# Kernel tuning notes

Hardware: AMD Instinct MI355X
Metric: run time of the kernel (lower is better)

Reference implementation:

```python
import jax, jax.numpy as jnp
import numpy as np

D_MODEL = 1024
NUM_HEADS = 16
DEPTH = D_MODEL // NUM_HEADS


def setup_inputs() -> dict:
    key = jax.random.key(0)
    ks = jax.random.split(key, 9)
    B, S = 2, 2048
    scale = 1.0 / np.sqrt(D_MODEL)
    x = jax.random.normal(ks[0], (B, S, D_MODEL), dtype=jnp.float32)
    wq = jax.random.normal(ks[1], (D_MODEL, D_MODEL), dtype=jnp.float32) * scale
    wk = jax.random.normal(ks[2], (D_MODEL, D_MODEL), dtype=jnp.float32) * scale
    wv = jax.random.normal(ks[3], (D_MODEL, D_MODEL), dtype=jnp.float32) * scale
    wo = jax.random.normal(ks[4], (D_MODEL, D_MODEL), dtype=jnp.float32) * scale
    bq = jnp.zeros((D_MODEL,), dtype=jnp.float32)
    bk = jnp.zeros((D_MODEL,), dtype=jnp.float32)
    bv = jnp.zeros((D_MODEL,), dtype=jnp.float32)
    bo = jnp.zeros((D_MODEL,), dtype=jnp.float32)
    return {"x": x, "wq": wq, "bq": bq, "wk": wk, "bk": bk,
            "wv": wv, "bv": bv, "wo": wo, "bo": bo}


def _split_heads(t):
    # [B, S, D] -> [B, H, S, depth]
    B, S, _ = t.shape
    return t.reshape(B, S, NUM_HEADS, DEPTH).transpose(0, 2, 1, 3)


def reference(x, wq, bq, wk, bk, wv, bv, wo, bo):
    q = _split_heads(x @ wq + bq)
    k = _split_heads(x @ wk + bk)
    v = _split_heads(x @ wv + bv)
    # scaled dot-product attention with materialized [B,H,S,S] scores
    logits = jnp.einsum("bhqd,bhkd->bhqk", q, k) / jnp.sqrt(
        jnp.asarray(DEPTH, dtype=x.dtype))
    attn = jax.nn.softmax(logits, axis=-1)
    out = jnp.einsum("bhqk,bhkd->bhqd", attn, v)
    B, _, S, _ = out.shape
    concat = out.transpose(0, 2, 1, 3).reshape(B, S, D_MODEL)
    return concat @ wo + bo
```

## Files before the change

kernel.cpp:

```cpp
#include <hip/hip_runtime.h>
#include <hip/hip_bf16.h>
#include <stdint.h>

typedef unsigned short u16;
typedef __attribute__((ext_vector_type(8))) short short8;
typedef __attribute__((ext_vector_type(4))) float f32x4;

__device__ __forceinline__ float bf2f(u16 u) {
    union { uint32_t u; float f; } v; v.u = ((uint32_t)u) << 16; return v.f;
}
__device__ __forceinline__ u16 f2bf(float f) {
    union { float f; uint32_t u; } v; v.f = f;
    uint32_t r = (v.u + 0x7fffu + ((v.u >> 16) & 1u)) >> 16;
    return (u16)r;
}
__device__ __forceinline__ uint32_t pkbf(float a, float b) {
    union { __hip_bfloat162 h; uint32_t w; } u;
    u.h = __float22bfloat162_rn(float2{a, b});
    return u.w;
}
__device__ __forceinline__ void store_out(u16* p, float v) { *p = f2bf(v); }
__device__ __forceinline__ void store_out(float* p, float v) { *p = v; }

__device__ __forceinline__ void async_ld16(const u16* g, u16* l) {
    __builtin_amdgcn_global_load_lds(
        (const __attribute__((address_space(1))) void*)g,
        (__attribute__((address_space(3))) void*)l, 16, 0, 0);
}

__global__ void prep(const float* __restrict__ x,
                     const float* __restrict__ w0, const float* __restrict__ w1,
                     const float* __restrict__ w2,
                     u16* __restrict__ xb, u16* __restrict__ wT) {
    const int z = blockIdx.z;
    __shared__ u16 tile[32][33];
    if (z >= 3) {
        int blk = (z - 3) * 1024 + blockIdx.y * 32 + blockIdx.x;
        int tid = threadIdx.y * 32 + threadIdx.x;
        int i = (blk * 256 + tid) * 8;
        float4 a = *(const float4*)(x + i);
        float4 b = *(const float4*)(x + i + 4);
        union { uint32_t w[4]; uint4 v; } o;
        o.w[0] = pkbf(a.x, a.y); o.w[1] = pkbf(a.z, a.w);
        o.w[2] = pkbf(b.x, b.y); o.w[3] = pkbf(b.z, b.w);
        *(uint4*)(xb + i) = o.v;
        return;
    }
    const float* in = (z == 0) ? w0 : (z == 1) ? w1 : w2;
    u16* o = wT + (size_t)z * 1024 * 1024;
    int xx = blockIdx.x * 32 + threadIdx.x;
    int y0 = blockIdx.y * 32;
#pragma unroll
    for (int j = threadIdx.y; j < 32; j += 8)
        tile[j][threadIdx.x] = f2bf(in[(size_t)(y0 + j) * 1024 + xx]);
    __syncthreads();
    int ox = blockIdx.y * 32 + threadIdx.x;
    int oy0 = blockIdx.x * 32;
#pragma unroll
    for (int j = threadIdx.y; j < 32; j += 8)
        o[(size_t)(oy0 + j) * 1024 + ox] = tile[threadIdx.x][j];
}

__global__ void transpose1(const float* __restrict__ w, u16* __restrict__ out) {
    __shared__ u16 tile[32][33];
    int x = blockIdx.x * 32 + threadIdx.x;
    int y0 = blockIdx.y * 32;
#pragma unroll
    for (int j = threadIdx.y; j < 32; j += 8)
        tile[j][threadIdx.x] = f2bf(w[(size_t)(y0 + j) * 1024 + x]);
    __syncthreads();
    int ox = blockIdx.y * 32 + threadIdx.x;
    int oy0 = blockIdx.x * 32;
#pragma unroll
    for (int j = threadIdx.y; j < 32; j += 8)
        out[(size_t)(oy0 + j) * 1024 + ox] = tile[threadIdx.x][j];
}

#define GBM 128
#define GBN 128
#define GBK 32

template <typename OutT>
__global__ __launch_bounds__(256) void gemm_bt(
    const u16* __restrict__ A, int lda,
    const u16* __restrict__ BT, int ldb,
    const float* __restrict__ bias0, const float* __restrict__ bias1,
    const float* __restrict__ bias2,
    OutT* __restrict__ C, int ldc, int K) {
    __shared__ __align__(16) u16 As[2][GBM * GBK];
    __shared__ __align__(16) u16 Bs[2][GBN * GBK];

    const int tid = threadIdx.x;
    const int wave = tid >> 6, lane = tid & 63;
    const int quad = lane >> 4, l16 = lane & 15;
    const int wr = wave >> 1, wc = wave & 1;

    int bx = blockIdx.x, by = blockIdx.y;
    if (gridDim.x == 24 && gridDim.y == 32) {
        const int wgid = blockIdx.x + blockIdx.y * 24;
        const int xcd = wgid & 7, t = wgid >> 3;
        bx = (xcd & 1) * 12 + t % 12;
        by = (xcd >> 1) * 8 + t / 12;
    }
    const int m0 = by * GBM, n0 = bx * GBN;

    const int seg = n0 >> 10;
    const float* bsel = (seg == 0) ? bias0 : (seg == 1) ? bias1 : bias2;

    f32x4 acc[4][4] = {};

    const int srow = tid >> 2;
    const int scol = (tid & 3) * 8;
    const u16* Ag0 = A + (size_t)(m0 + srow) * lda + scol;
    const u16* Ag1 = Ag0 + (size_t)64 * lda;
    const u16* Bg0 = BT + (size_t)(n0 + srow) * ldb + scol;
    const u16* Bg1 = Bg0 + (size_t)64 * ldb;
    const int woff = wave << 9;

    async_ld16(Ag0, As[0] + woff);
    async_ld16(Ag1, As[0] + woff + 64 * GBK);
    async_ld16(Bg0, Bs[0] + woff);
    async_ld16(Bg1, Bs[0] + woff + 64 * GBK);

    int cur = 0;
    for (int kb = 0; kb < K; kb += GBK) {
        __syncthreads();

        if (kb + GBK < K) {
            const int nxt = cur ^ 1;
            async_ld16(Ag0 + kb + GBK, As[nxt] + woff);
            async_ld16(Ag1 + kb + GBK, As[nxt] + woff + 64 * GBK);
            async_ld16(Bg0 + kb + GBK, Bs[nxt] + woff);
            async_ld16(Bg1 + kb + GBK, Bs[nxt] + woff + 64 * GBK);
        }

        short8 af[4], bf[4];
#pragma unroll
        for (int mt = 0; mt < 4; mt++)
            af[mt] = *(const short8*)(As[cur] + (wr * 64 + mt * 16 + l16) * GBK + quad * 8);
#pragma unroll
        for (int nt = 0; nt < 4; nt++)
            bf[nt] = *(const short8*)(Bs[cur] + (wc * 64 + nt * 16 + l16) * GBK + quad * 8);
#pragma unroll
        for (int mt = 0; mt < 4; mt++)
#pragma unroll
            for (int nt = 0; nt < 4; nt++)
                acc[mt][nt] = __builtin_amdgcn_mfma_f32_16x16x32_bf16(
                    af[mt], bf[nt], acc[mt][nt], 0, 0, 0);
        cur ^= 1;
    }

#pragma unroll
    for (int nt = 0; nt < 4; nt++) {
        int col = n0 + wc * 64 + nt * 16 + l16;
        float bv = bsel[col & 1023];
#pragma unroll
        for (int mt = 0; mt < 4; mt++) {
            int row = m0 + wr * 64 + mt * 16 + quad * 4;
#pragma unroll
            for (int r = 0; r < 4; r++)
                store_out(&C[(size_t)(row + r) * ldc + col], acc[mt][nt][r] + bv);
        }
    }
}

__global__ __launch_bounds__(256) void gemm_bt64(
    const u16* __restrict__ A, int lda,
    const u16* __restrict__ BT, int ldb,
    const float* __restrict__ bias,
    float* __restrict__ C, int ldc, int K) {
    __shared__ __align__(16) u16 As[2][64 * GBK];
    __shared__ __align__(16) u16 Bs[2][128 * GBK];

    const int tid = threadIdx.x;
    const int wave = tid >> 6, lane = tid & 63;
    const int quad = lane >> 4, l16 = lane & 15;

    int bx = blockIdx.x, by = blockIdx.y;
    if (gridDim.x == 8 && gridDim.y == 64) {
        const int wgid = blockIdx.x + blockIdx.y * 8;
        const int xcd = wgid & 7, t = wgid >> 3;
        bx = t & 7;
        by = (xcd << 3) + (t >> 3);
    }
    const int m0 = by * 64, n0 = bx * 128;

    f32x4 acc[4][2] = {};

    const int srow = tid >> 2;
    const int scol = (tid & 3) * 8;
    const u16* Ag0 = A + (size_t)(m0 + srow) * lda + scol;
    const u16* Bg0 = BT + (size_t)(n0 + srow) * ldb + scol;
    const u16* Bg1 = Bg0 + (size_t)64 * ldb;
    const int woff = wave << 9;

    async_ld16(Ag0, As[0] + woff);
    async_ld16(Bg0, Bs[0] + woff);
    async_ld16(Bg1, Bs[0] + woff + 64 * GBK);

    int cur = 0;
    for (int kb = 0; kb < K; kb += GBK) {
        __syncthreads();

        if (kb + GBK < K) {
            const int nxt = cur ^ 1;
            async_ld16(Ag0 + kb + GBK, As[nxt] + woff);
            async_ld16(Bg0 + kb + GBK, Bs[nxt] + woff);
            async_ld16(Bg1 + kb + GBK, Bs[nxt] + woff + 64 * GBK);
        }

        short8 af[4], bf[2];
#pragma unroll
        for (int mt = 0; mt < 4; mt++)
            af[mt] = *(const short8*)(As[cur] + (mt * 16 + l16) * GBK + quad * 8);
#pragma unroll
        for (int nt = 0; nt < 2; nt++)
            bf[nt] = *(const short8*)(Bs[cur] + (wave * 32 + nt * 16 + l16) * GBK + quad * 8);
#pragma unroll
        for (int mt = 0; mt < 4; mt++)
#pragma unroll
            for (int nt = 0; nt < 2; nt++)
                acc[mt][nt] = __builtin_amdgcn_mfma_f32_16x16x32_bf16(
                    af[mt], bf[nt], acc[mt][nt], 0, 0, 0);
        cur ^= 1;
    }

#pragma unroll
    for (int nt = 0; nt < 2; nt++) {
        int col = n0 + wave * 32 + nt * 16 + l16;
        float bv = bias[col & 1023];
#pragma unroll
        for (int mt = 0; mt < 4; mt++) {
            int row = m0 + mt * 16 + quad * 4;
#pragma unroll
            for (int r = 0; r < 4; r++)
                C[(size_t)(row + r) * ldc + col] = acc[mt][nt][r] + bv;
        }
    }
}

#define SEQ 2048
#define BQT 128
#define BKV 128
#define LDK 72
#define LDKV 136

__global__ __launch_bounds__(256) void attn(u16* __restrict__ QKV) {
    __shared__ __align__(16) u16 Ks[BKV * LDK];
    __shared__ __align__(16) u16 Vs[64 * LDKV];

    const int tid = threadIdx.x;
    const int wave = tid >> 6, lane = tid & 63;
    const int quad = lane >> 4, l16 = lane & 15;
    const int h = blockIdx.y, bb = blockIdx.z;
    const int q0 = blockIdx.x * BQT;
    const size_t tok0 = (size_t)bb * SEQ;

    const u16* Qb = QKV + tok0 * 3072 + h * 64;
    const u16* Kb = QKV + tok0 * 3072 + 1024 + h * 64;
    const u16* Vb = QKV + tok0 * 3072 + 2048 + h * 64;

    const float cs = 0.18033688011112042f;

    int qr[2];
    qr[0] = q0 + wave * 16 + l16;
    qr[1] = qr[0] + 64;
    short8 aq[2][2];
#pragma unroll
    for (int s = 0; s < 2; s++) {
        union { short8 v; u16 u[8]; uint32_t w[4]; } qa, qb;
        qa.v = *(const short8*)(Qb + (size_t)qr[s] * 3072 + quad * 8);
        qb.v = *(const short8*)(Qb + (size_t)qr[s] * 3072 + 32 + quad * 8);
#pragma unroll
        for (int j = 0; j < 4; j++) {
            qa.w[j] = pkbf(bf2f(qa.u[2 * j]) * cs, bf2f(qa.u[2 * j + 1]) * cs);
            qb.w[j] = pkbf(bf2f(qb.u[2 * j]) * cs, bf2f(qb.u[2 * j + 1]) * cs);
        }
        aq[s][0] = qa.v; aq[s][1] = qb.v;
    }

    f32x4 o[2][4] = {};
    f32x4 o_l[2] = {};

    const short8 vone = {16256, 16256, 16256, 16256,
                         16256, 16256, 16256, 16256};

    const int srow = tid >> 2;
    const int scc = (tid & 3) * 16;
    const int pr = tid & 63;
    const int dg = wave;

    const u16* kg = Kb + (size_t)srow * 3072 + scc;
    const u16* vg = Vb + (size_t)(2 * pr) * 3072 + dg * 16;

    const int kvb = 2 * pr;
    const int kvp = (kvb & 96) | (((kvb >> 2) & 3) << 3) |
                    (((kvb >> 4) & 1) << 2) | (kvb & 3);

    uint4 k0r = *(const uint4*)(kg);
    uint4 k1r = *(const uint4*)(kg + 8);
    uint4 k2r = *(const uint4*)(kg + (size_t)64 * 3072);
    uint4 k3r = *(const uint4*)(kg + (size_t)64 * 3072 + 8);
    uint4 va0 = *(const uint4*)(vg);
    uint4 va1 = *(const uint4*)(vg + 8);
    uint4 vb0 = *(const uint4*)(vg + 3072);
    uint4 vb1 = *(const uint4*)(vg + 3072 + 8);

    for (int j0 = 0; j0 < SEQ; j0 += BKV) {
        *(uint4*)(Ks + srow * LDK + scc) = k0r;
        *(uint4*)(Ks + srow * LDK + scc + 8) = k1r;
        *(uint4*)(Ks + (srow + 64) * LDK + scc) = k2r;
        *(uint4*)(Ks + (srow + 64) * LDK + scc + 8) = k3r;
        {
            union { uint4 v[2]; u16 u[16]; } a, b;
            a.v[0] = va0; a.v[1] = va1; b.v[0] = vb0; b.v[1] = vb1;
#pragma unroll
            for (int j = 0; j < 16; j++) {
                uint32_t w = (uint32_t)a.u[j] | ((uint32_t)b.u[j] << 16);
                *(uint32_t*)(Vs + (dg * 16 + j) * LDKV + kvp) = w;
            }
        }
        __syncthreads();

        if (j0 + BKV < SEQ) {
            size_t off = (size_t)(j0 + BKV) * 3072;
            k0r = *(const uint4*)(kg + off);
            k1r = *(const uint4*)(kg + off + 8);
            k2r = *(const uint4*)(kg + off + (size_t)64 * 3072);
            k3r = *(const uint4*)(kg + off + (size_t)64 * 3072 + 8);
            va0 = *(const uint4*)(vg + off);
            va1 = *(const uint4*)(vg + off + 8);
            vb0 = *(const uint4*)(vg + off + 3072);
            vb1 = *(const uint4*)(vg + off + 3072 + 8);
        }

        f32x4 st[2][8];
#pragma unroll
        for (int kkt = 0; kkt < 8; kkt++) {
            f32x4 s0 = {}, s1 = {};
#pragma unroll
            for (int k2 = 0; k2 < 2; k2++) {
                short8 ak = *(const short8*)(Ks + (kkt * 16 + l16) * LDK + k2 * 32 + quad * 8);
                s0 = __builtin_amdgcn_mfma_f32_16x16x32_bf16(ak, aq[0][k2], s0, 0, 0, 0);
                s1 = __builtin_amdgcn_mfma_f32_16x16x32_bf16(ak, aq[1][k2], s1, 0, 0, 0);
            }
            st[0][kkt] = s0; st[1][kkt] = s1;
        }

#pragma unroll
        for (int s = 0; s < 2; s++)
#pragma unroll
            for (int kkt = 0; kkt < 8; kkt++)
#pragma unroll
                for (int r = 0; r < 4; r++)
                    st[s][kkt][r] = __builtin_amdgcn_exp2f(st[s][kkt][r]);

#pragma unroll
        for (int tt = 0; tt < 4; tt++) {
            union { uint32_t w[4]; short8 v; } bp0, bp1;
            bp0.w[0] = pkbf(st[0][2 * tt][0], st[0][2 * tt][1]);
            bp0.w[1] = pkbf(st[0][2 * tt][2], st[0][2 * tt][3]);
            bp0.w[2] = pkbf(st[0][2 * tt + 1][0], st[0][2 * tt + 1][1]);
            bp0.w[3] = pkbf(st[0][2 * tt + 1][2], st[0][2 * tt + 1][3]);
            bp1.w[0] = pkbf(st[1][2 * tt][0], st[1][2 * tt][1]);
            bp1.w[1] = pkbf(st[1][2 * tt][2], st[1][2 * tt][3]);
            bp1.w[2] = pkbf(st[1][2 * tt + 1][0], st[1][2 * tt + 1][1]);
            bp1.w[3] = pkbf(st[1][2 * tt + 1][2], st[1][2 * tt + 1][3]);

            o_l[0] = __builtin_amdgcn_mfma_f32_16x16x32_bf16(vone, bp0.v, o_l[0], 0, 0, 0);
            o_l[1] = __builtin_amdgcn_mfma_f32_16x16x32_bf16(vone, bp1.v, o_l[1], 0, 0, 0);
#pragma unroll
            for (int dt = 0; dt < 4; dt++) {
                short8 av = *(const short8*)(Vs + (dt * 16 + l16) * LDKV +
                                             tt * 32 + quad * 8);
                o[0][dt] = __builtin_amdgcn_mfma_f32_16x16x32_bf16(av, bp0.v, o[0][dt], 0, 0, 0);
                o[1][dt] = __builtin_amdgcn_mfma_f32_16x16x32_bf16(av, bp1.v, o[1][dt], 0, 0, 0);
            }
        }

        __syncthreads();
    }

#pragma unroll
    for (int s = 0; s < 2; s++) {
        const float inv_l = 1.0f / o_l[s][0];
        u16* orow = QKV + (tok0 + qr[s]) * 3072 + h * 64;
#pragma unroll
        for (int dt = 0; dt < 4; dt++) {
            uint32_t w0 = pkbf(o[s][dt][0] * inv_l, o[s][dt][1] * inv_l);
            uint32_t w1 = pkbf(o[s][dt][2] * inv_l, o[s][dt][3] * inv_l);
            uint2 w = {w0, w1};
            *(uint2*)(orow + dt * 16 + quad * 4) = w;
        }
    }
}

extern "C" void kernel_launch(void* const* d_in, const int* in_sizes, int n_in,
                              void* d_out, int out_size, void* d_ws, size_t ws_size,
                              hipStream_t stream) {
    const float* x  = (const float*)d_in[0];
    const float* wq = (const float*)d_in[1];
    const float* bq = (const float*)d_in[2];
    const float* wk = (const float*)d_in[3];
    const float* bk = (const float*)d_in[4];
    const float* wv = (const float*)d_in[5];
    const float* bv = (const float*)d_in[6];
    const float* wo = (const float*)d_in[7];
    const float* bo = (const float*)d_in[8];
    (void)in_sizes; (void)n_in; (void)out_size; (void)ws_size;

    u16* QKV = (u16*)d_ws;
    u16* wT  = QKV + (size_t)4096 * 3072;
    u16* xb  = wT + (size_t)3 * 1024 * 1024;
    u16* woT = xb;

    prep<<<dim3(32, 32, 5), dim3(32, 8), 0, stream>>>(x, wq, wk, wv, xb, wT);
    gemm_bt<u16><<<dim3(24, 32), 256, 0, stream>>>(xb, 1024, wT, 1024, bq, bk, bv,
                                                   QKV, 3072, 1024);
    transpose1<<<dim3(32, 32), dim3(32, 8), 0, stream>>>(wo, woT);
    attn<<<dim3(16, 16, 2), 256, 0, stream>>>(QKV);
    gemm_bt64<<<dim3(8, 64), 256, 0, stream>>>(QKV, 3072, woT, 1024, bo,
                                               (float*)d_out, 1024, 1024);
}
```

Baseline: 200.7 us.

## Split attention block across 8 waves with one query tile per wave

The attention kernel now launches 512 threads per block, and each of the 8 waves owns a single 16-row query tile instead of two. K/V staging is spread across twice as many threads, so each thread loads half as much. The aim is more waves in flight to hide MFMA and exp latency, with fewer registers per thread. In exchange each K/V tile held in LDS is reused by fewer query tiles per wave, and the per-thread instruction-level parallelism drops.

```diff
diff --git a/kernel.cpp b/kernel.cpp
--- a/kernel.cpp
+++ b/kernel.cpp
@@ -245,7 +245,7 @@
 #define LDK 72
 #define LDKV 136
 
-__global__ __launch_bounds__(256) void attn(u16* __restrict__ QKV) {
+__global__ __launch_bounds__(512, 2) void attn(u16* __restrict__ QKV) {
     __shared__ __align__(16) u16 Ks[BKV * LDK];
     __shared__ __align__(16) u16 Vs[64 * LDKV];
 
@@ -262,36 +262,32 @@
 
     const float cs = 0.18033688011112042f;
 
-    int qr[2];
-    qr[0] = q0 + wave * 16 + l16;
-    qr[1] = qr[0] + 64;
-    short8 aq[2][2];
-#pragma unroll
-    for (int s = 0; s < 2; s++) {
+    const int qr = q0 + wave * 16 + l16;
+    short8 aq[2];
+    {
         union { short8 v; u16 u[8]; uint32_t w[4]; } qa, qb;
-        qa.v = *(const short8*)(Qb + (size_t)qr[s] * 3072 + quad * 8);
-        qb.v = *(const short8*)(Qb + (size_t)qr[s] * 3072 + 32 + quad * 8);
+        qa.v = *(const short8*)(Qb + (size_t)qr * 3072 + quad * 8);
+        qb.v = *(const short8*)(Qb + (size_t)qr * 3072 + 32 + quad * 8);
 #pragma unroll
         for (int j = 0; j < 4; j++) {
             qa.w[j] = pkbf(bf2f(qa.u[2 * j]) * cs, bf2f(qa.u[2 * j + 1]) * cs);
             qb.w[j] = pkbf(bf2f(qb.u[2 * j]) * cs, bf2f(qb.u[2 * j + 1]) * cs);
         }
-        aq[s][0] = qa.v; aq[s][1] = qb.v;
-    }
-
-    f32x4 o[2][4] = {};
-    f32x4 o_l[2] = {};
+        aq[0] = qa.v; aq[1] = qb.v;
+    }
+
+    f32x4 o[4] = {};
+    f32x4 o_l = {};
 
     const short8 vone = {16256, 16256, 16256, 16256,
                          16256, 16256, 16256, 16256};
 
     const int srow = tid >> 2;
     const int scc = (tid & 3) * 16;
-    const int pr = tid & 63;
-    const int dg = wave;
-
+    const int pr = lane;
+    const int dgv = wave;
     const u16* kg = Kb + (size_t)srow * 3072 + scc;
-    const u16* vg = Vb + (size_t)(2 * pr) * 3072 + dg * 16;
+    const u16* vg = Vb + (size_t)(2 * pr) * 3072 + dgv * 8;
 
     const int kvb = 2 * pr;
     const int kvp = (kvb & 96) | (((kvb >> 2) & 3) << 3) |
@@ -299,25 +295,19 @@
 
     uint4 k0r = *(const uint4*)(kg);
     uint4 k1r = *(const uint4*)(kg + 8);
-    uint4 k2r = *(const uint4*)(kg + (size_t)64 * 3072);
-    uint4 k3r = *(const uint4*)(kg + (size_t)64 * 3072 + 8);
     uint4 va0 = *(const uint4*)(vg);
-    uint4 va1 = *(const uint4*)(vg + 8);
     uint4 vb0 = *(const uint4*)(vg + 3072);
-    uint4 vb1 = *(const uint4*)(vg + 3072 + 8);
 
     for (int j0 = 0; j0 < SEQ; j0 += BKV) {
         *(uint4*)(Ks + srow * LDK + scc) = k0r;
         *(uint4*)(Ks + srow * LDK + scc + 8) = k1r;
-        *(uint4*)(Ks + (srow + 64) * LDK + scc) = k2r;
-        *(uint4*)(Ks + (srow + 64) * LDK + scc + 8) = k3r;
         {
-            union { uint4 v[2]; u16 u[16]; } a, b;
-            a.v[0] = va0; a.v[1] = va1; b.v[0] = vb0; b.v[1] = vb1;
-#pragma unroll
-            for (int j = 0; j < 16; j++) {
+            union { uint4 v; u16 u[8]; } a, b;
+            a.v = va0; b.v = vb0;
+#pragma unroll
+            for (int j = 0; j < 8; j++) {
                 uint32_t w = (uint32_t)a.u[j] | ((uint32_t)b.u[j] << 16);
-                *(uint32_t*)(Vs + (dg * 16 + j) * LDKV + kvp) = w;
+                *(uint32_t*)(Vs + (dgv * 8 + j) * LDKV + kvp) = w;
             }
         }
         __syncthreads();
@@ -326,69 +316,55 @@
             size_t off = (size_t)(j0 + BKV) * 3072;
             k0r = *(const uint4*)(kg + off);
             k1r = *(const uint4*)(kg + off + 8);
-            k2r = *(const uint4*)(kg + off + (size_t)64 * 3072);
-            k3r = *(const uint4*)(kg + off + (size_t)64 * 3072 + 8);
             va0 = *(const uint4*)(vg + off);
-            va1 = *(const uint4*)(vg + off + 8);
             vb0 = *(const uint4*)(vg + off + 3072);
-            vb1 = *(const uint4*)(vg + off + 3072 + 8);
-        }
-
-        f32x4 st[2][8];
+        }
+
+        f32x4 st[8];
 #pragma unroll
         for (int kkt = 0; kkt < 8; kkt++) {
-            f32x4 s0 = {}, s1 = {};
+            f32x4 s0 = {};
 #pragma unroll
             for (int k2 = 0; k2 < 2; k2++) {
                 short8 ak = *(const short8*)(Ks + (kkt * 16 + l16) * LDK + k2 * 32 + quad * 8);
-                s0 = __builtin_amdgcn_mfma_f32_16x16x32_bf16(ak, aq[0][k2], s0, 0, 0, 0);
-                s1 = __builtin_amdgcn_mfma_f32_16x16x32_bf16(ak, aq[1][k2], s1, 0, 0, 0);
+                s0 = __builtin_amdgcn_mfma_f32_16x16x32_bf16(ak, aq[k2], s0, 0, 0, 0);
             }
-            st[0][kkt] = s0; st[1][kkt] = s1;
-        }
-
-#pragma unroll
-        for (int s = 0; s < 2; s++)
-#pragma unroll
-            for (int kkt = 0; kkt < 8; kkt++)
-#pragma unroll
-                for (int r = 0; r < 4; r++)
-                    st[s][kkt][r] = __builtin_amdgcn_exp2f(st[s][kkt][r]);
+            st[kkt] = s0;
+        }
+
+#pragma unroll
+        for (int kkt = 0; kkt < 8; kkt++)
+#pragma unroll
+            for (int r = 0; r < 4; r++)
+                st[kkt][r] = __builtin_amdgcn_exp2f(st[kkt][r]);
 
 #pragma unroll
         for (int tt = 0; tt < 4; tt++) {
-            union { uint32_t w[4]; short8 v; } bp0, bp1;
-            bp0.w[0] = pkbf(st[0][2 * tt][0], st[0][2 * tt][1]);
-            bp0.w[1] = pkbf(st[0][2 * tt][2], st[0][2 * tt][3]);
-            bp0.w[2] = pkbf(st[0][2 * tt + 1][0], st[0][2 * tt + 1][1]);
-            bp0.w[3] = pkbf(st[0][2 * tt + 1][2], st[0][2 * tt + 1][3]);
-            bp1.w[0] = pkbf(st[1][2 * tt][0], st[1][2 * tt][1]);
-            bp1.w[1] = pkbf(st[1][2 * tt][2], st[1][2 * tt][3]);
-            bp1.w[2] = pkbf(st[1][2 * tt + 1][0], st[1][2 * tt + 1][1]);
-            bp1.w[3] = pkbf(st[1][2 * tt + 1][2], st[1][2 * tt + 1][3]);
-
-            o_l[0] = __builtin_amdgcn_mfma_f32_16x16x32_bf16(vone, bp0.v, o_l[0], 0, 0, 0);
-            o_l[1] = __builtin_amdgcn_mfma_f32_16x16x32_bf16(vone, bp1.v, o_l[1], 0, 0, 0);
+            union { uint32_t w[4]; short8 v; } bp;
+            bp.w[0] = pkbf(st[2 * tt][0], st[2 * tt][1]);
+            bp.w[1] = pkbf(st[2 * tt][2], st[2 * tt][3]);
+            bp.w[2] = pkbf(st[2 * tt + 1][0], st[2 * tt + 1][1]);
+            bp.w[3] = pkbf(st[2 * tt + 1][2], st[2 * tt + 1][3]);
+
+            o_l = __builtin_amdgcn_mfma_f32_16x16x32_bf16(vone, bp.v, o_l, 0, 0, 0);
 #pragma unroll
             for (int dt = 0; dt < 4; dt++) {
                 short8 av = *(const short8*)(Vs + (dt * 16 + l16) * LDKV +
                                              tt * 32 + quad * 8);
-                o[0][dt] = __builtin_amdgcn_mfma_f32_16x16x32_bf16(av, bp0.v, o[0][dt], 0, 0, 0);
-                o[1][dt] = __builtin_amdgcn_mfma_f32_16x16x32_bf16(av, bp1.v, o[1][dt], 0, 0, 0);
+                o[dt] = __builtin_amdgcn_mfma_f32_16x16x32_bf16(av, bp.v, o[dt], 0, 0, 0);
             }
         }
 
         __syncthreads();
     }
 
-#pragma unroll
-    for (int s = 0; s < 2; s++) {
-        const float inv_l = 1.0f / o_l[s][0];
-        u16* orow = QKV + (tok0 + qr[s]) * 3072 + h * 64;
+    {
+        const float inv_l = 1.0f / o_l[0];
+        u16* orow = QKV + (tok0 + qr) * 3072 + h * 64;
 #pragma unroll
         for (int dt = 0; dt < 4; dt++) {
-            uint32_t w0 = pkbf(o[s][dt][0] * inv_l, o[s][dt][1] * inv_l);
-            uint32_t w1 = pkbf(o[s][dt][2] * inv_l, o[s][dt][3] * inv_l);
+            uint32_t w0 = pkbf(o[dt][0] * inv_l, o[dt][1] * inv_l);
+            uint32_t w1 = pkbf(o[dt][2] * inv_l, o[dt][3] * inv_l);
             uint2 w = {w0, w1};
             *(uint2*)(orow + dt * 16 + quad * 4) = w;
         }
@@ -418,7 +394,7 @@
     gemm_bt<u16><<<dim3(24, 32), 256, 0, stream>>>(xb, 1024, wT, 1024, bq, bk, bv,
                                                    QKV, 3072, 1024);
     transpose1<<<dim3(32, 32), dim3(32, 8), 0, stream>>>(wo, woT);
-    attn<<<dim3(16, 16, 2), 256, 0, stream>>>(QKV);
+    attn<<<dim3(16, 16, 2), 512, 0, stream>>>(QKV);
     gemm_bt64<<<dim3(8, 64), 256, 0, stream>>>(QKV, 3072, woT, 1024, bo,
                                                (float*)d_out, 1024, 1024);
 }
```

Result: no change. 201.9 us (+0.6%).

## Double-buffer K/V shared tiles to drop one barrier per iteration

Applied to the files above, without the earlier changes.

Splits the K and V shared-memory tiles into two buffers. Each iteration computes on the current buffer, then writes the prefetched next tile into the other buffer, so only one __syncthreads per iteration is needed instead of two. This doubles LDS use per block, from about 35KB to about 70KB, which may reduce occupancy. The prefetched registers now stay live across the whole compute phase, which raises register pressure.

```diff
diff --git a/kernel.cpp b/kernel.cpp
--- a/kernel.cpp
+++ b/kernel.cpp
@@ -246,8 +246,8 @@
 #define LDKV 136
 
 __global__ __launch_bounds__(256) void attn(u16* __restrict__ QKV) {
-    __shared__ __align__(16) u16 Ks[BKV * LDK];
-    __shared__ __align__(16) u16 Vs[64 * LDKV];
+    __shared__ __align__(16) u16 Ks[2][BKV * LDK];
+    __shared__ __align__(16) u16 Vs[2][64 * LDKV];
 
     const int tid = threadIdx.x;
     const int wave = tid >> 6, lane = tid & 63;
@@ -297,32 +297,33 @@
     const int kvp = (kvb & 96) | (((kvb >> 2) & 3) << 3) |
                     (((kvb >> 4) & 1) << 2) | (kvb & 3);
 
-    uint4 k0r = *(const uint4*)(kg);
-    uint4 k1r = *(const uint4*)(kg + 8);
-    uint4 k2r = *(const uint4*)(kg + (size_t)64 * 3072);
-    uint4 k3r = *(const uint4*)(kg + (size_t)64 * 3072 + 8);
-    uint4 va0 = *(const uint4*)(vg);
-    uint4 va1 = *(const uint4*)(vg + 8);
-    uint4 vb0 = *(const uint4*)(vg + 3072);
-    uint4 vb1 = *(const uint4*)(vg + 3072 + 8);
-
+    {
+        uint4 k0r = *(const uint4*)(kg);
+        uint4 k1r = *(const uint4*)(kg + 8);
+        uint4 k2r = *(const uint4*)(kg + (size_t)64 * 3072);
+        uint4 k3r = *(const uint4*)(kg + (size_t)64 * 3072 + 8);
+        *(uint4*)(Ks[0] + srow * LDK + scc) = k0r;
+        *(uint4*)(Ks[0] + srow * LDK + scc + 8) = k1r;
+        *(uint4*)(Ks[0] + (srow + 64) * LDK + scc) = k2r;
+        *(uint4*)(Ks[0] + (srow + 64) * LDK + scc + 8) = k3r;
+        union { uint4 v[2]; u16 u[16]; } a, b;
+        a.v[0] = *(const uint4*)(vg);
+        a.v[1] = *(const uint4*)(vg + 8);
+        b.v[0] = *(const uint4*)(vg + 3072);
+        b.v[1] = *(const uint4*)(vg + 3072 + 8);
+#pragma unroll
+        for (int j = 0; j < 16; j++) {
+            uint32_t w = (uint32_t)a.u[j] | ((uint32_t)b.u[j] << 16);
+            *(uint32_t*)(Vs[0] + (dg * 16 + j) * LDKV + kvp) = w;
+        }
+    }
+    __syncthreads();
+
+    int cur = 0;
     for (int j0 = 0; j0 < SEQ; j0 += BKV) {
-        *(uint4*)(Ks + srow * LDK + scc) = k0r;
-        *(uint4*)(Ks + srow * LDK + scc + 8) = k1r;
-        *(uint4*)(Ks + (srow + 64) * LDK + scc) = k2r;
-        *(uint4*)(Ks + (srow + 64) * LDK + scc + 8) = k3r;
-        {
-            union { uint4 v[2]; u16 u[16]; } a, b;
-            a.v[0] = va0; a.v[1] = va1; b.v[0] = vb0; b.v[1] = vb1;
-#pragma unroll
-            for (int j = 0; j < 16; j++) {
-                uint32_t w = (uint32_t)a.u[j] | ((uint32_t)b.u[j] << 16);
-                *(uint32_t*)(Vs + (dg * 16 + j) * LDKV + kvp) = w;
-            }
-        }
-        __syncthreads();
-
-        if (j0 + BKV < SEQ) {
+        const bool more = (j0 + BKV < SEQ);
+        uint4 k0r, k1r, k2r, k3r, va0, va1, vb0, vb1;
+        if (more) {
             size_t off = (size_t)(j0 + BKV) * 3072;
             k0r = *(const uint4*)(kg + off);
             k1r = *(const uint4*)(kg + off + 8);
@@ -334,13 +335,16 @@
             vb1 = *(const uint4*)(vg + off + 3072 + 8);
         }
 
+        const u16* Ksc = Ks[cur];
+        const u16* Vsc = Vs[cur];
+
         f32x4 st[2][8];
 #pragma unroll
         for (int kkt = 0; kkt < 8; kkt++) {
             f32x4 s0 = {}, s1 = {};
 #pragma unroll
             for (int k2 = 0; k2 < 2; k2++) {
-                short8 ak = *(const short8*)(Ks + (kkt * 16 + l16) * LDK + k2 * 32 + quad * 8);
+                short8 ak = *(const short8*)(Ksc + (kkt * 16 + l16) * LDK + k2 * 32 + quad * 8);
                 s0 = __builtin_amdgcn_mfma_f32_16x16x32_bf16(ak, aq[0][k2], s0, 0, 0, 0);
                 s1 = __builtin_amdgcn_mfma_f32_16x16x32_bf16(ak, aq[1][k2], s1, 0, 0, 0);
             }
@@ -371,14 +375,30 @@
             o_l[1] = __builtin_amdgcn_mfma_f32_16x16x32_bf16(vone, bp1.v, o_l[1], 0, 0, 0);
 #pragma unroll
             for (int dt = 0; dt < 4; dt++) {
-                short8 av = *(const short8*)(Vs + (dt * 16 + l16) * LDKV +
+                short8 av = *(const short8*)(Vsc + (dt * 16 + l16) * LDKV +
                                              tt * 32 + quad * 8);
                 o[0][dt] = __builtin_amdgcn_mfma_f32_16x16x32_bf16(av, bp0.v, o[0][dt], 0, 0, 0);
                 o[1][dt] = __builtin_amdgcn_mfma_f32_16x16x32_bf16(av, bp1.v, o[1][dt], 0, 0, 0);
             }
         }
 
+        if (more) {
+            const int nxt = cur ^ 1;
+            *(uint4*)(Ks[nxt] + srow * LDK + scc) = k0r;
+            *(uint4*)(Ks[nxt] + srow * LDK + scc + 8) = k1r;
+            *(uint4*)(Ks[nxt] + (srow + 64) * LDK + scc) = k2r;
+            *(uint4*)(Ks[nxt] + (srow + 64) * LDK + scc + 8) = k3r;
+            union { uint4 v[2]; u16 u[16]; } a, b;
+            a.v[0] = va0; a.v[1] = va1; b.v[0] = vb0; b.v[1] = vb1;
+#pragma unroll
+            for (int j = 0; j < 16; j++) {
+                uint32_t w = (uint32_t)a.u[j] | ((uint32_t)b.u[j] << 16);
+                *(uint32_t*)(Vs[nxt] + (dg * 16 + j) * LDKV + kvp) = w;
+            }
+        }
+
         __syncthreads();
+        cur ^= 1;
     }
 
 #pragma unroll
```

Result: no change. 203.5 us (+1.4%).
